# Kernel tuning notes

Hardware: AMD Instinct MI355X
Metric: run time of the kernel (lower is better)

The kernel has to match this reference:

```python
import jax, jax.numpy as jnp
import numpy as np

PADDED_NODE_ID = -1
B, N, F = 4096, 128, 64


def setup_inputs() -> dict:
    key = jax.random.key(0)
    k1, k2, k3, k4, k5, k6 = jax.random.split(key, 6)
    src_ids = jax.random.randint(k1, (B, N), 0, 1000, dtype=jnp.int64 if jax.config.jax_enable_x64 else jnp.int32)
    dst_ids = jax.random.randint(k2, (B, N), 0, 1000, dtype=src_ids.dtype)
    w1 = jax.random.normal(k3, (F, 1), dtype=jnp.float32) * 0.1
    b1 = jax.random.normal(k4, (F,), dtype=jnp.float32) * 0.1
    w2 = jax.random.normal(k5, (F, F), dtype=jnp.float32) * 0.1
    b2 = jax.random.normal(k6, (F,), dtype=jnp.float32) * 0.1
    return {"src_neighbour_nodes_ids": src_ids, "dst_neighbour_nodes_ids": dst_ids,
            "w1": w1, "b1": b1, "w2": w2, "b2": b2}


def _pairwise_count(a, b):
    # count[b, i] = #{ j : a[b, i] == b[b, j] }  -- batched histogram via equality
    eq = a[:, :, None] == b[:, None, :]  # [B, N, N] bool
    return eq.sum(axis=-1).astype(jnp.float32)


def _mlp(freq, w1, b1, w2, b2):
    # freq: [B, N, 2] -> Linear(1,F) -> ReLU -> Linear(F,F), then sum over dim 2
    h = freq[..., None] * w1[:, 0] + b1          # [B, N, 2, F]
    h = jax.nn.relu(h)
    out = jnp.einsum('bncf,gf->bncg', h, w2) + b2  # [B, N, 2, F]
    return out.sum(axis=2)                        # [B, N, F]


def reference(src_neighbour_nodes_ids, dst_neighbour_nodes_ids, w1, b1, w2, b2):
    src, dst = src_neighbour_nodes_ids, dst_neighbour_nodes_ids
    src_in_src = _pairwise_count(src, src)
    dst_in_dst = _pairwise_count(dst, dst)
    src_in_dst = _pairwise_count(src, dst)
    dst_in_src = _pairwise_count(dst, src)

    src_pad = (src == PADDED_NODE_ID)[..., None]
    dst_pad = (dst == PADDED_NODE_ID)[..., None]
    source_freq = jnp.where(src_pad, 0.0, jnp.stack([src_in_src, src_in_dst], axis=-1))  # [B,N,2]
    dst_freq = jnp.where(dst_pad, 0.0, jnp.stack([dst_in_dst, dst_in_src], axis=-1))      # [B,N,2]

    src_feat = _mlp(source_freq, w1, b1, w2, b2)
    dst_feat = _mlp(dst_freq, w1, b1, w2, b2)
    return src_feat, dst_feat
```

## Files before the change

kernel.cpp:

```cpp
#include <hip/hip_runtime.h>

#define BATCH 4096
#define NN 128
#define FF 64
#define NC 129
#define HIST 1000
#define NTAB 16
#define TSTRIDE 68
#define ROWS_PER_BLK 512
#define TOTAL_ROWS (2 * BATCH * NN)
#define CNT_WS_OFF 65536

__global__ void build_table_kernel(const float* __restrict__ w1,
                                   const float* __restrict__ b1,
                                   const float* __restrict__ w2,
                                   const float* __restrict__ b2,
                                   float* __restrict__ table) {
    int c = blockIdx.x;
    int g = threadIdx.x;
    float cf = (float)c;
    float acc = b2[g];
    #pragma unroll
    for (int f = 0; f < FF; ++f) {
        float h = cf * w1[f] + b1[f];
        h = h > 0.0f ? h : 0.0f;
        acc += h * w2[g * FF + f];
    }
    table[c * FF + g] = acc;
}

__global__ __launch_bounds__(256, 8)
void count_kernel(const int* __restrict__ src,
                  const int* __restrict__ dst,
                  unsigned* __restrict__ cnt) {
    __shared__ unsigned s_hist[HIST];

    const int b   = blockIdx.x;
    const int tid = threadIdx.x;

    const int my = (tid < NN) ? src[b * NN + tid] : dst[b * NN + (tid - NN)];
    const unsigned inc = (tid < NN) ? 1u : 0x10000u;
    const bool valid = (my >= 0) && (my < HIST);

    #pragma unroll
    for (int i = tid; i < HIST; i += 256) s_hist[i] = 0u;
    __syncthreads();

    if (valid) atomicAdd(&s_hist[my], inc);
    __syncthreads();

    const unsigned packed = valid ? s_hist[my] : 0u;
    const int n = (tid < NN) ? tid : (tid - NN);
    const int buf = (tid < NN) ? 0 : 1;
    cnt[(size_t)buf * BATCH * NN + (size_t)b * NN + n] = packed;
}

__global__ __launch_bounds__(256, 8)
void emit_kernel(const unsigned* __restrict__ cnt,
                 const float* __restrict__ table,
                 float* __restrict__ out) {
    __shared__ float    s_tab[NTAB * TSTRIDE];
    __shared__ unsigned s_c[ROWS_PER_BLK];

    const int bb  = blockIdx.x;
    const int tid = threadIdx.x;
    const size_t row0 = (size_t)bb * ROWS_PER_BLK;

    {
        const int r = tid >> 4, c = tid & 15;
        *(float4*)&s_tab[r * TSTRIDE + c * 4] = ((const float4*)table)[r * (FF / 4) + c];
    }
    s_c[tid]       = cnt[row0 + tid];
    s_c[tid + 256] = cnt[row0 + tid + 256];
    __syncthreads();

    const float4* __restrict__ tab4 = (const float4*)table;
    float4* __restrict__ out4 = (float4*)out + row0 * (FF / 4);

    #pragma unroll 4
    for (int it = 0; it < (ROWS_PER_BLK * (FF / 4)) / 256; ++it) {
        const int idx = it * 256 + tid;
        const int row = idx >> 4;
        const int g4  = idx & 15;
        const unsigned h  = s_c[row];
        const unsigned c0 = h & 0xffffu;
        const unsigned c1 = h >> 16;
        float4 v0 = *(const float4*)&s_tab[(c0 & (NTAB - 1)) * TSTRIDE + g4 * 4];
        float4 v1 = *(const float4*)&s_tab[(c1 & (NTAB - 1)) * TSTRIDE + g4 * 4];
        if (__builtin_expect((h & 0xfff0fff0u) != 0u, 0)) {
            v0 = tab4[c0 * (FF / 4) + g4];
            v1 = tab4[c1 * (FF / 4) + g4];
        }
        float4 r;
        r.x = v0.x + v1.x; r.y = v0.y + v1.y;
        r.z = v0.z + v1.z; r.w = v0.w + v1.w;
        out4[idx] = r;
    }
}

extern "C" void kernel_launch(void* const* d_in, const int* in_sizes, int n_in,
                              void* d_out, int out_size, void* d_ws, size_t ws_size,
                              hipStream_t stream) {
    const int*   src = (const int*)d_in[0];
    const int*   dst = (const int*)d_in[1];
    const float* w1  = (const float*)d_in[2];
    const float* b1  = (const float*)d_in[3];
    const float* w2  = (const float*)d_in[4];
    const float* b2  = (const float*)d_in[5];
    float* out   = (float*)d_out;
    float* table = (float*)d_ws;
    unsigned* cnt = (unsigned*)((char*)d_ws + CNT_WS_OFF);

    build_table_kernel<<<NC, FF, 0, stream>>>(w1, b1, w2, b2, table);
    count_kernel<<<BATCH, 256, 0, stream>>>(src, dst, cnt);
    emit_kernel<<<TOTAL_ROWS / ROWS_PER_BLK, 256, 0, stream>>>(cnt, table, out);
}
```

Before: 276.0 us.

## Fuse histogram counting and table-lookup emission into one kernel

Merges the count and emit kernels into a single kernel that processes two batches per block. Counts stay in shared memory instead of going through a global workspace, which removes one kernel launch and the global write and read of the packed counts. The fused kernel uses more shared memory per block and adds extra barriers. The histogram phase may also reduce overlap with the store-heavy emit phase.

```diff
diff --git a/kernel.cpp b/kernel.cpp
--- a/kernel.cpp
+++ b/kernel.cpp
@@ -7,9 +7,8 @@
 #define HIST 1000
 #define NTAB 16
 #define TSTRIDE 68
-#define ROWS_PER_BLK 512
-#define TOTAL_ROWS (2 * BATCH * NN)
-#define CNT_WS_OFF 65536
+#define BPB 2
+#define PADDED_ID (-1)
 
 __global__ void build_table_kernel(const float* __restrict__ w1,
                                    const float* __restrict__ b1,
@@ -30,71 +29,77 @@
 }
 
 __global__ __launch_bounds__(256, 8)
-void count_kernel(const int* __restrict__ src,
+void fused_kernel(const int* __restrict__ src,
                   const int* __restrict__ dst,
-                  unsigned* __restrict__ cnt) {
-    __shared__ unsigned s_hist[HIST];
-
-    const int b   = blockIdx.x;
-    const int tid = threadIdx.x;
-
-    const int my = (tid < NN) ? src[b * NN + tid] : dst[b * NN + (tid - NN)];
-    const unsigned inc = (tid < NN) ? 1u : 0x10000u;
-    const bool valid = (my >= 0) && (my < HIST);
-
-    #pragma unroll
-    for (int i = tid; i < HIST; i += 256) s_hist[i] = 0u;
-    __syncthreads();
-
-    if (valid) atomicAdd(&s_hist[my], inc);
-    __syncthreads();
-
-    const unsigned packed = valid ? s_hist[my] : 0u;
-    const int n = (tid < NN) ? tid : (tid - NN);
-    const int buf = (tid < NN) ? 0 : 1;
-    cnt[(size_t)buf * BATCH * NN + (size_t)b * NN + n] = packed;
-}
-
-__global__ __launch_bounds__(256, 8)
-void emit_kernel(const unsigned* __restrict__ cnt,
-                 const float* __restrict__ table,
-                 float* __restrict__ out) {
+                  const float* __restrict__ table,
+                  float* __restrict__ out) {
+    __shared__ unsigned s_hist[BPB * HIST];
+    __shared__ unsigned s_cnt[BPB * 256];
     __shared__ float    s_tab[NTAB * TSTRIDE];
-    __shared__ unsigned s_c[ROWS_PER_BLK];
 
     const int bb  = blockIdx.x;
+    const int b0  = bb * BPB;
     const int tid = threadIdx.x;
-    const size_t row0 = (size_t)bb * ROWS_PER_BLK;
 
     {
         const int r = tid >> 4, c = tid & 15;
         *(float4*)&s_tab[r * TSTRIDE + c * 4] = ((const float4*)table)[r * (FF / 4) + c];
     }
-    s_c[tid]       = cnt[row0 + tid];
-    s_c[tid + 256] = cnt[row0 + tid + 256];
+
+    int my[BPB];
+    #pragma unroll
+    for (int q = 0; q < BPB; ++q)
+        my[q] = (tid < NN) ? src[(size_t)(b0 + q) * NN + tid]
+                           : dst[(size_t)(b0 + q) * NN + (tid - NN)];
+    const unsigned inc = (tid < NN) ? 1u : 0x10000u;
+
+    #pragma unroll
+    for (int i = tid; i < BPB * HIST; i += 256) s_hist[i] = 0u;
+    __syncthreads();
+
+    #pragma unroll
+    for (int q = 0; q < BPB; ++q) {
+        const int m = my[q];
+        if (m >= 0 && m < HIST) atomicAdd(&s_hist[q * HIST + m], inc);
+    }
+    __syncthreads();
+
+    #pragma unroll
+    for (int q = 0; q < BPB; ++q) {
+        const int m = my[q];
+        s_cnt[q * 256 + tid] = (m >= 0 && m < HIST) ? s_hist[q * HIST + m] : 0u;
+    }
     __syncthreads();
 
     const float4* __restrict__ tab4 = (const float4*)table;
-    float4* __restrict__ out4 = (float4*)out + row0 * (FF / 4);
+    float4* __restrict__ o0 = (float4*)out + (size_t)b0 * NN * (FF / 4);
+    float4* __restrict__ o1 = o0 + (size_t)BATCH * NN * (FF / 4);
 
-    #pragma unroll 4
-    for (int it = 0; it < (ROWS_PER_BLK * (FF / 4)) / 256; ++it) {
-        const int idx = it * 256 + tid;
-        const int row = idx >> 4;
-        const int g4  = idx & 15;
-        const unsigned h  = s_c[row];
-        const unsigned c0 = h & 0xffffu;
-        const unsigned c1 = h >> 16;
-        float4 v0 = *(const float4*)&s_tab[(c0 & (NTAB - 1)) * TSTRIDE + g4 * 4];
-        float4 v1 = *(const float4*)&s_tab[(c1 & (NTAB - 1)) * TSTRIDE + g4 * 4];
-        if (__builtin_expect((h & 0xfff0fff0u) != 0u, 0)) {
-            v0 = tab4[c0 * (FF / 4) + g4];
-            v1 = tab4[c1 * (FF / 4) + g4];
+    #pragma unroll
+    for (int half = 0; half < 2; ++half) {
+        float4* __restrict__ o = half ? o1 : o0;
+        const int roff = half ? NN : 0;
+        #pragma unroll 4
+        for (int it = 0; it < (BPB * NN * (FF / 4)) / 256; ++it) {
+            const int idx = it * 256 + tid;
+            const int row = idx >> 4;
+            const int g4  = idx & 15;
+            const int q   = row >> 7;
+            const int n   = row & (NN - 1);
+            const unsigned h  = s_cnt[q * 256 + roff + n];
+            const unsigned c0 = h & 0xffffu;
+            const unsigned c1 = h >> 16;
+            float4 v0 = *(const float4*)&s_tab[(c0 & (NTAB - 1)) * TSTRIDE + g4 * 4];
+            float4 v1 = *(const float4*)&s_tab[(c1 & (NTAB - 1)) * TSTRIDE + g4 * 4];
+            if (__builtin_expect((h & 0xfff0fff0u) != 0u, 0)) {
+                v0 = tab4[c0 * (FF / 4) + g4];
+                v1 = tab4[c1 * (FF / 4) + g4];
+            }
+            float4 r;
+            r.x = v0.x + v1.x; r.y = v0.y + v1.y;
+            r.z = v0.z + v1.z; r.w = v0.w + v1.w;
+            o[idx] = r;
         }
-        float4 r;
-        r.x = v0.x + v1.x; r.y = v0.y + v1.y;
-        r.z = v0.z + v1.z; r.w = v0.w + v1.w;
-        out4[idx] = r;
     }
 }
 
@@ -109,9 +114,7 @@
     const float* b2  = (const float*)d_in[5];
     float* out   = (float*)d_out;
     float* table = (float*)d_ws;
-    unsigned* cnt = (unsigned*)((char*)d_ws + CNT_WS_OFF);
 
     build_table_kernel<<<NC, FF, 0, stream>>>(w1, b1, w2, b2, table);
-    count_kernel<<<BATCH, 256, 0, stream>>>(src, dst, cnt);
-    emit_kernel<<<TOTAL_ROWS / ROWS_PER_BLK, 256, 0, stream>>>(cnt, table, out);
+    fused_kernel<<<BATCH / BPB, 256, 0, stream>>>(src, dst, table, out);
 }
```

Result: no change. 272.4 us (-1.3%).
